# Kernel optimization log

Measured on AMD Instinct MI355X. Metric: run time of the kernel, lower is better.

## Reference

```python
import jax, jax.numpy as jnp
import numpy as np

D_MODEL = 128
NUM_HEADS = 8
LN_EPS = 1e-5


def setup_inputs() -> dict:
    key = jax.random.key(0)
    ks = jax.random.split(key, 12)
    B, T, D = 4, 2048, D_MODEL
    s = 1.0 / np.sqrt(D)
    return {
        "queries": jax.random.normal(ks[0], (B, T, D), jnp.float32),
        "keys": jax.random.normal(ks[1], (B, T, D), jnp.float32),
        "values": jax.random.normal(ks[2], (B, T, D), jnp.float32),
        "Wq": jax.random.normal(ks[3], (D, D), jnp.float32) * s,
        "bq": jnp.zeros((D,), jnp.float32),
        "Wk": jax.random.normal(ks[4], (D, D), jnp.float32) * s,
        "bk": jnp.zeros((D,), jnp.float32),
        "Wv": jax.random.normal(ks[5], (D, D), jnp.float32) * s,
        "bv": jnp.zeros((D,), jnp.float32),
        "Wo": jax.random.normal(ks[6], (D, D), jnp.float32) * s,
        "bo": jnp.zeros((D,), jnp.float32),
        "gamma": jnp.ones((D,), jnp.float32),
        "beta": jnp.zeros((D,), jnp.float32),
    }


def reference(queries, keys, values, Wq, bq, Wk, bk, Wv, bv, Wo, bo, gamma, beta):
    B, T, D = queries.shape
    H = NUM_HEADS
    dk = D // H

    def split_heads(x):  # [B,T,D] -> [B,H,T,dk]
        return x.reshape(B, -1, H, dk).transpose(0, 2, 1, 3)

    Q = split_heads(queries @ Wq + bq)
    K = split_heads(keys @ Wk + bk)
    V = split_heads(values @ Wv + bv)

    scale = 1.0 / jnp.sqrt(jnp.asarray(dk, jnp.float32))
    scores = jnp.einsum("bhqd,bhkd->bhqk", Q, K) * scale  # [B,H,T,T]
    attn = jax.nn.softmax(scores, axis=-1)
    ctx = jnp.einsum("bhqk,bhkd->bhqd", attn, V)  # [B,H,T,dk]

    out = ctx.transpose(0, 2, 1, 3).reshape(B, T, D)  # combine heads
    out = out @ Wo + bo

    x = out + queries  # residual
    mean = jnp.mean(x, axis=-1, keepdims=True)
    var = jnp.mean((x - mean) ** 2, axis=-1, keepdims=True)
    out = (x - mean) / jnp.sqrt(var + LN_EPS) * gamma + beta
    return out, attn
```

## Files before the change

### kernel.cpp

```cpp
#include <hip/hip_runtime.h>

#define B_ 4
#define T_ 2048
#define D_ 128
#define H_ 8
#define DK_ 16

typedef __attribute__((ext_vector_type(8))) short short8;
typedef __attribute__((ext_vector_type(4))) float floatx4;

__device__ __forceinline__ short f2bf(float x) {
    unsigned u = __builtin_bit_cast(unsigned, x);
    u += 0x7FFFu + ((u >> 16) & 1u);
    return (short)(u >> 16);
}

__device__ __forceinline__ unsigned cvt_pk_bf16(float lo, float hi) {
    unsigned r;
    asm("v_cvt_pk_bf16_f32 %0, %1, %2" : "=v"(r) : "v"(lo), "v"(hi));
    return r;
}

__global__ __launch_bounds__(64) void qkv_kernel(
    const float* __restrict__ q_in, const float* __restrict__ k_in,
    const float* __restrict__ v_in,
    const float* __restrict__ Wq, const float* __restrict__ bq,
    const float* __restrict__ Wk, const float* __restrict__ bk,
    const float* __restrict__ Wv, const float* __restrict__ bv,
    short* __restrict__ q_ws, short* __restrict__ k_ws, short* __restrict__ vt_ws)
{
    int mat = blockIdx.x >> 9;
    int rb  = blockIdx.x & 511;
    int row0 = rb * 16;
    int b  = row0 >> 11;
    int t0 = row0 & (T_ - 1);

    const float* X    = (mat == 0) ? q_in : (mat == 1) ? k_in : v_in;
    const float* W    = (mat == 0) ? Wq   : (mat == 1) ? Wk   : Wv;
    const float* bias = (mat == 0) ? bq   : (mat == 1) ? bk   : bv;

    __shared__ float xt[16][128];
    int tid = threadIdx.x;
    #pragma unroll
    for (int i = 0; i < 8; ++i) {
        int idx = tid + i * 64;
        int r = idx >> 5, c4 = idx & 31;
        *(float4*)&xt[r][c4 * 4] =
            *(const float4*)&X[(size_t)(row0 + r) * 128 + c4 * 4];
    }
    __syncthreads();

    int c0 = tid, c1 = tid + 64;
    float accA[16], accB[16];
    float b0 = bias[c0], b1 = bias[c1];
    #pragma unroll
    for (int r = 0; r < 16; ++r) { accA[r] = b0; accB[r] = b1; }

    for (int d4 = 0; d4 < 32; ++d4) {
        float w0[4], w1[4];
        #pragma unroll
        for (int j = 0; j < 4; ++j) {
            w0[j] = W[(d4 * 4 + j) * 128 + c0];
            w1[j] = W[(d4 * 4 + j) * 128 + c1];
        }
        #pragma unroll
        for (int r = 0; r < 16; ++r) {
            float4 xv = *(const float4*)&xt[r][d4 * 4];
            accA[r] += xv.x * w0[0] + xv.y * w0[1] + xv.z * w0[2] + xv.w * w0[3];
            accB[r] += xv.x * w1[0] + xv.y * w1[1] + xv.z * w1[2] + xv.w * w1[3];
        }
    }

    int hA = c0 >> 4, dA = c0 & 15;
    int hB = c1 >> 4, dB = c1 & 15;
    #pragma unroll
    for (int r = 0; r < 16; ++r) {
        int t = t0 + r;
        float vA = accA[r], vB = accB[r];
        if (mat == 0) { vA *= 0.25f; vB *= 0.25f; }
        if (mat == 2) {
            vt_ws[((size_t)(b * H_ + hA) * DK_ + dA) * T_ + t] = f2bf(vA);
            vt_ws[((size_t)(b * H_ + hB) * DK_ + dB) * T_ + t] = f2bf(vB);
        } else {
            short* dst = (mat == 0) ? q_ws : k_ws;
            dst[((size_t)(b * H_ + hA) * T_ + t) * DK_ + dA] = f2bf(vA);
            dst[((size_t)(b * H_ + hB) * T_ + t) * DK_ + dB] = f2bf(vB);
        }
    }
}

__global__ __launch_bounds__(512) void attn_kernel(
    const short* __restrict__ q_ws, const short* __restrict__ k_ws,
    const short* __restrict__ vt_ws,
    float* __restrict__ attn, float* __restrict__ ctx_ws)
{
    __shared__ __align__(16) short klds[T_ * DK_];
    __shared__ __align__(16) short vtlds[DK_ * (T_ + 8)];
    __shared__ __align__(16) short tblds[8 * 16 * 40];

    int tid = threadIdx.x;
    int bh = blockIdx.x >> 3;
    int qc = blockIdx.x & 7;
    int b = bh >> 3, h = bh & 7;

    const short* kbase  = k_ws  + (size_t)bh * T_ * DK_;
    const short* vtbase = vt_ws + (size_t)bh * DK_ * T_;

    #pragma unroll
    for (int i = 0; i < 8; ++i) {
        int idx = tid + i * 512;
        *(short8*)&klds[idx * 8] = *(const short8*)&kbase[idx * 8];
    }
    #pragma unroll
    for (int i = 0; i < 8; ++i) {
        int idx = tid + i * 512;
        int d = idx >> 8, off = idx & 255;
        *(short8*)&vtlds[d * (T_ + 8) + off * 8] =
            *(const short8*)&vtbase[d * T_ + off * 8];
    }
    __syncthreads();

    int wid = tid >> 6, lane = tid & 63;
    int l15 = lane & 15, quad = lane >> 4;
    int half8 = (quad & 1) * 8;
    short8 z8 = {0, 0, 0, 0, 0, 0, 0, 0};

    float* attn_bh = attn + (size_t)bh * T_ * T_;

    for (int tt = 0; tt < 2; ++tt) {
        int qrow0 = qc * 256 + tt * 128 + wid * 16;

        short8 bq = *(const short8*)
            &q_ws[((size_t)bh * T_ + qrow0 + l15) * DK_ + half8];
        if (quad >= 2) bq = z8;

        float lsum = 0.f;
        for (int tk0 = 0; tk0 < T_; tk0 += 32) {
            short8 ak0 = *(const short8*)&klds[(tk0 + l15) * DK_ + half8];
            short8 ak1 = *(const short8*)&klds[(tk0 + 16 + l15) * DK_ + half8];
            if (quad >= 2) { ak0 = z8; ak1 = z8; }
            floatx4 s0 = __builtin_amdgcn_mfma_f32_16x16x32_bf16(
                ak0, bq, (floatx4){0.f, 0.f, 0.f, 0.f}, 0, 0, 0);
            floatx4 s1 = __builtin_amdgcn_mfma_f32_16x16x32_bf16(
                ak1, bq, (floatx4){0.f, 0.f, 0.f, 0.f}, 0, 0, 0);
            #pragma unroll
            for (int r = 0; r < 4; ++r)
                lsum += __expf(s0[r]) + __expf(s1[r]);
        }
        lsum += __shfl_xor(lsum, 16);
        lsum += __shfl_xor(lsum, 32);
        float inv = 1.0f / lsum;

        short* tb = &tblds[wid * 16 * 40];
        floatx4 ctx = {0.f, 0.f, 0.f, 0.f};
        float* ap = attn_bh + (size_t)(qrow0 + l15) * T_;

        for (int tk0 = 0; tk0 < T_; tk0 += 32) {
            short8 ak0 = *(const short8*)&klds[(tk0 + l15) * DK_ + half8];
            short8 ak1 = *(const short8*)&klds[(tk0 + 16 + l15) * DK_ + half8];
            if (quad >= 2) { ak0 = z8; ak1 = z8; }
            floatx4 s0 = __builtin_amdgcn_mfma_f32_16x16x32_bf16(
                ak0, bq, (floatx4){0.f, 0.f, 0.f, 0.f}, 0, 0, 0);
            floatx4 s1 = __builtin_amdgcn_mfma_f32_16x16x32_bf16(
                ak1, bq, (floatx4){0.f, 0.f, 0.f, 0.f}, 0, 0, 0);

            float p0[4], p1[4];
            #pragma unroll
            for (int r = 0; r < 4; ++r) {
                p0[r] = __expf(s0[r]) * inv;
                p1[r] = __expf(s1[r]) * inv;
            }
            *(float4*)(ap + tk0 + quad * 4) =
                make_float4(p0[0], p0[1], p0[2], p0[3]);
            *(float4*)(ap + tk0 + 16 + quad * 4) =
                make_float4(p1[0], p1[1], p1[2], p1[3]);

            unsigned u0 = cvt_pk_bf16(p0[0], p0[1]);
            unsigned u1 = cvt_pk_bf16(p0[2], p0[3]);
            unsigned u2 = cvt_pk_bf16(p1[0], p1[1]);
            unsigned u3 = cvt_pk_bf16(p1[2], p1[3]);
            uint2 w01 = {u0, u1}, w23 = {u2, u3};
            *(uint2*)&tb[l15 * 40 + quad * 4]      = w01;
            *(uint2*)&tb[l15 * 40 + 16 + quad * 4] = w23;

            short8 pa = *(const short8*)&tb[l15 * 40 + quad * 8];
            short8 vb = *(const short8*)&vtlds[l15 * (T_ + 8) + tk0 + quad * 8];
            ctx = __builtin_amdgcn_mfma_f32_16x16x32_bf16(pa, vb, ctx, 0, 0, 0);
        }
        #pragma unroll
        for (int r = 0; r < 4; ++r)
            ctx_ws[((size_t)b * T_ + qrow0 + quad * 4 + r) * D_ + h * DK_ + l15] =
                ctx[r];
    }
}

__global__ __launch_bounds__(256) void outln_kernel(
    const float* __restrict__ ctx_ws, const float* __restrict__ Wo,
    const float* __restrict__ bo, const float* __restrict__ q_in,
    const float* __restrict__ gamma, const float* __restrict__ beta,
    float* __restrict__ out)
{
    __shared__ float xrow[4][4][128];
    int tid = threadIdx.x, wid = tid >> 6, lane = tid & 63;
    int row0 = blockIdx.x * 16 + wid * 4;

    #pragma unroll
    for (int r = 0; r < 4; ++r) {
        xrow[wid][r][lane]      = ctx_ws[(size_t)(row0 + r) * 128 + lane];
        xrow[wid][r][lane + 64] = ctx_ws[(size_t)(row0 + r) * 128 + lane + 64];
    }

    float acc0[4], acc1[4];
    float bb0 = bo[lane], bb1 = bo[lane + 64];
    #pragma unroll
    for (int r = 0; r < 4; ++r) { acc0[r] = bb0; acc1[r] = bb1; }

    for (int d4 = 0; d4 < 32; ++d4) {
        float w0[4], w1[4];
        #pragma unroll
        for (int j = 0; j < 4; ++j) {
            w0[j] = Wo[(d4 * 4 + j) * 128 + lane];
            w1[j] = Wo[(d4 * 4 + j) * 128 + lane + 64];
        }
        #pragma unroll
        for (int r = 0; r < 4; ++r) {
            float4 xv = *(const float4*)&xrow[wid][r][d4 * 4];
            acc0[r] += xv.x * w0[0] + xv.y * w0[1] + xv.z * w0[2] + xv.w * w0[3];
            acc1[r] += xv.x * w1[0] + xv.y * w1[1] + xv.z * w1[2] + xv.w * w1[3];
        }
    }

    float g0 = gamma[lane], g1 = gamma[lane + 64];
    float be0 = beta[lane], be1 = beta[lane + 64];
    #pragma unroll
    for (int r = 0; r < 4; ++r) {
        size_t row = row0 + r;
        float x0 = acc0[r] + q_in[row * 128 + lane];
        float x1 = acc1[r] + q_in[row * 128 + lane + 64];
        float s = x0 + x1, s2 = x0 * x0 + x1 * x1;
        #pragma unroll
        for (int off = 1; off < 64; off <<= 1) {
            s  += __shfl_xor(s, off);
            s2 += __shfl_xor(s2, off);
        }
        float mean = s * (1.0f / 128.0f);
        float var  = s2 * (1.0f / 128.0f) - mean * mean;
        float rstd = rsqrtf(var + 1e-5f);
        out[row * 128 + lane]      = (x0 - mean) * rstd * g0 + be0;
        out[row * 128 + lane + 64] = (x1 - mean) * rstd * g1 + be1;
    }
}

extern "C" void kernel_launch(void* const* d_in, const int* in_sizes, int n_in,
                              void* d_out, int out_size, void* d_ws, size_t ws_size,
                              hipStream_t stream)
{
    const float* queries = (const float*)d_in[0];
    const float* keys    = (const float*)d_in[1];
    const float* values  = (const float*)d_in[2];
    const float* Wq = (const float*)d_in[3];  const float* bq = (const float*)d_in[4];
    const float* Wk = (const float*)d_in[5];  const float* bk = (const float*)d_in[6];
    const float* Wv = (const float*)d_in[7];  const float* bv = (const float*)d_in[8];
    const float* Wo = (const float*)d_in[9];  const float* bo = (const float*)d_in[10];
    const float* gamma = (const float*)d_in[11];
    const float* beta  = (const float*)d_in[12];

    short* q_ws  = (short*)d_ws;
    short* k_ws  = q_ws  + (1 << 20);
    short* vt_ws = k_ws  + (1 << 20);
    float* ctx_ws = (float*)(vt_ws + (1 << 20));

    float* out  = (float*)d_out;
    float* attn = out + (size_t)B_ * T_ * D_;

    qkv_kernel<<<dim3(3 * 512), dim3(64), 0, stream>>>(
        queries, keys, values, Wq, bq, Wk, bk, Wv, bv, q_ws, k_ws, vt_ws);
    attn_kernel<<<dim3(256), dim3(512), 0, stream>>>(
        q_ws, k_ws, vt_ws, attn, ctx_ws);
    outln_kernel<<<dim3(512), dim3(256), 0, stream>>>(
        ctx_ws, Wo, bo, queries, gamma, beta, out);
}
```

Measured before the change: 623.9 us.

## Drop LDS K/V staging, double grid, swizzle blocks, use nontemporal attn stores

Removes the per-block copy of K and V^T into LDS (about 130 KB) and reads K/V straight from global memory, relying on L2/cache reuse. The grid doubles to 512 blocks with one 128-row query tile each, and launch bounds ask for 4 blocks per CU to raise occupancy. Block IDs are swizzled so neighbouring blocks spread across heads, and the large attention-matrix writes use nontemporal stores to limit cache pollution. The risk is more global/L2 traffic and load latency in the inner loops in exchange for higher occupancy.

```diff
diff --git a/kernel.cpp b/kernel.cpp
--- a/kernel.cpp
+++ b/kernel.cpp
@@ -89,36 +89,22 @@
     }
 }
 
-__global__ __launch_bounds__(512) void attn_kernel(
+__global__ __launch_bounds__(512, 4) void attn_kernel(
     const short* __restrict__ q_ws, const short* __restrict__ k_ws,
     const short* __restrict__ vt_ws,
     float* __restrict__ attn, float* __restrict__ ctx_ws)
 {
-    __shared__ __align__(16) short klds[T_ * DK_];
-    __shared__ __align__(16) short vtlds[DK_ * (T_ + 8)];
     __shared__ __align__(16) short tblds[8 * 16 * 40];
 
     int tid = threadIdx.x;
-    int bh = blockIdx.x >> 3;
-    int qc = blockIdx.x & 7;
+    int bid = blockIdx.x;
+    int wg  = ((bid & 7) << 6) | (bid >> 3);
+    int bh = wg >> 4;
+    int qc = wg & 15;
     int b = bh >> 3, h = bh & 7;
 
     const short* kbase  = k_ws  + (size_t)bh * T_ * DK_;
     const short* vtbase = vt_ws + (size_t)bh * DK_ * T_;
-
-    #pragma unroll
-    for (int i = 0; i < 8; ++i) {
-        int idx = tid + i * 512;
-        *(short8*)&klds[idx * 8] = *(const short8*)&kbase[idx * 8];
-    }
-    #pragma unroll
-    for (int i = 0; i < 8; ++i) {
-        int idx = tid + i * 512;
-        int d = idx >> 8, off = idx & 255;
-        *(short8*)&vtlds[d * (T_ + 8) + off * 8] =
-            *(const short8*)&vtbase[d * T_ + off * 8];
-    }
-    __syncthreads();
 
     int wid = tid >> 6, lane = tid & 63;
     int l15 = lane & 15, quad = lane >> 4;
@@ -126,72 +112,71 @@
     short8 z8 = {0, 0, 0, 0, 0, 0, 0, 0};
 
     float* attn_bh = attn + (size_t)bh * T_ * T_;
-
-    for (int tt = 0; tt < 2; ++tt) {
-        int qrow0 = qc * 256 + tt * 128 + wid * 16;
-
-        short8 bq = *(const short8*)
-            &q_ws[((size_t)bh * T_ + qrow0 + l15) * DK_ + half8];
-        if (quad >= 2) bq = z8;
-
-        float lsum = 0.f;
-        for (int tk0 = 0; tk0 < T_; tk0 += 32) {
-            short8 ak0 = *(const short8*)&klds[(tk0 + l15) * DK_ + half8];
-            short8 ak1 = *(const short8*)&klds[(tk0 + 16 + l15) * DK_ + half8];
-            if (quad >= 2) { ak0 = z8; ak1 = z8; }
-            floatx4 s0 = __builtin_amdgcn_mfma_f32_16x16x32_bf16(
-                ak0, bq, (floatx4){0.f, 0.f, 0.f, 0.f}, 0, 0, 0);
-            floatx4 s1 = __builtin_amdgcn_mfma_f32_16x16x32_bf16(
-                ak1, bq, (floatx4){0.f, 0.f, 0.f, 0.f}, 0, 0, 0);
-            #pragma unroll
-            for (int r = 0; r < 4; ++r)
-                lsum += __expf(s0[r]) + __expf(s1[r]);
-        }
-        lsum += __shfl_xor(lsum, 16);
-        lsum += __shfl_xor(lsum, 32);
-        float inv = 1.0f / lsum;
-
-        short* tb = &tblds[wid * 16 * 40];
-        floatx4 ctx = {0.f, 0.f, 0.f, 0.f};
-        float* ap = attn_bh + (size_t)(qrow0 + l15) * T_;
-
-        for (int tk0 = 0; tk0 < T_; tk0 += 32) {
-            short8 ak0 = *(const short8*)&klds[(tk0 + l15) * DK_ + half8];
-            short8 ak1 = *(const short8*)&klds[(tk0 + 16 + l15) * DK_ + half8];
-            if (quad >= 2) { ak0 = z8; ak1 = z8; }
-            floatx4 s0 = __builtin_amdgcn_mfma_f32_16x16x32_bf16(
-                ak0, bq, (floatx4){0.f, 0.f, 0.f, 0.f}, 0, 0, 0);
-            floatx4 s1 = __builtin_amdgcn_mfma_f32_16x16x32_bf16(
-                ak1, bq, (floatx4){0.f, 0.f, 0.f, 0.f}, 0, 0, 0);
-
-            float p0[4], p1[4];
-            #pragma unroll
-            for (int r = 0; r < 4; ++r) {
-                p0[r] = __expf(s0[r]) * inv;
-                p1[r] = __expf(s1[r]) * inv;
-            }
-            *(float4*)(ap + tk0 + quad * 4) =
-                make_float4(p0[0], p0[1], p0[2], p0[3]);
-            *(float4*)(ap + tk0 + 16 + quad * 4) =
-                make_float4(p1[0], p1[1], p1[2], p1[3]);
-
-            unsigned u0 = cvt_pk_bf16(p0[0], p0[1]);
-            unsigned u1 = cvt_pk_bf16(p0[2], p0[3]);
-            unsigned u2 = cvt_pk_bf16(p1[0], p1[1]);
-            unsigned u3 = cvt_pk_bf16(p1[2], p1[3]);
-            uint2 w01 = {u0, u1}, w23 = {u2, u3};
-            *(uint2*)&tb[l15 * 40 + quad * 4]      = w01;
-            *(uint2*)&tb[l15 * 40 + 16 + quad * 4] = w23;
-
-            short8 pa = *(const short8*)&tb[l15 * 40 + quad * 8];
-            short8 vb = *(const short8*)&vtlds[l15 * (T_ + 8) + tk0 + quad * 8];
-            ctx = __builtin_amdgcn_mfma_f32_16x16x32_bf16(pa, vb, ctx, 0, 0, 0);
-        }
+    int qrow0 = qc * 128 + wid * 16;
+
+    short8 bq = *(const short8*)
+        &q_ws[((size_t)bh * T_ + qrow0 + l15) * DK_ + half8];
+    if (quad >= 2) bq = z8;
+
+    float lsum = 0.f;
+    #pragma unroll 2
+    for (int tk0 = 0; tk0 < T_; tk0 += 32) {
+        short8 ak0 = *(const short8*)&kbase[(tk0 + l15) * DK_ + half8];
+        short8 ak1 = *(const short8*)&kbase[(tk0 + 16 + l15) * DK_ + half8];
+        if (quad >= 2) { ak0 = z8; ak1 = z8; }
+        floatx4 s0 = __builtin_amdgcn_mfma_f32_16x16x32_bf16(
+            ak0, bq, (floatx4){0.f, 0.f, 0.f, 0.f}, 0, 0, 0);
+        floatx4 s1 = __builtin_amdgcn_mfma_f32_16x16x32_bf16(
+            ak1, bq, (floatx4){0.f, 0.f, 0.f, 0.f}, 0, 0, 0);
         #pragma unroll
         for (int r = 0; r < 4; ++r)
-            ctx_ws[((size_t)b * T_ + qrow0 + quad * 4 + r) * D_ + h * DK_ + l15] =
-                ctx[r];
-    }
+            lsum += __expf(s0[r]) + __expf(s1[r]);
+    }
+    lsum += __shfl_xor(lsum, 16);
+    lsum += __shfl_xor(lsum, 32);
+    float inv = 1.0f / lsum;
+
+    short* tb = &tblds[wid * 16 * 40];
+    floatx4 ctx = {0.f, 0.f, 0.f, 0.f};
+    float* ap = attn_bh + (size_t)(qrow0 + l15) * T_;
+
+    #pragma unroll 2
+    for (int tk0 = 0; tk0 < T_; tk0 += 32) {
+        short8 ak0 = *(const short8*)&kbase[(tk0 + l15) * DK_ + half8];
+        short8 ak1 = *(const short8*)&kbase[(tk0 + 16 + l15) * DK_ + half8];
+        if (quad >= 2) { ak0 = z8; ak1 = z8; }
+        floatx4 s0 = __builtin_amdgcn_mfma_f32_16x16x32_bf16(
+            ak0, bq, (floatx4){0.f, 0.f, 0.f, 0.f}, 0, 0, 0);
+        floatx4 s1 = __builtin_amdgcn_mfma_f32_16x16x32_bf16(
+            ak1, bq, (floatx4){0.f, 0.f, 0.f, 0.f}, 0, 0, 0);
+
+        float p0[4], p1[4];
+        #pragma unroll
+        for (int r = 0; r < 4; ++r) {
+            p0[r] = __expf(s0[r]) * inv;
+            p1[r] = __expf(s1[r]) * inv;
+        }
+        floatx4 v0 = {p0[0], p0[1], p0[2], p0[3]};
+        floatx4 v1 = {p1[0], p1[1], p1[2], p1[3]};
+        __builtin_nontemporal_store(v0, (floatx4*)(ap + tk0 + quad * 4));
+        __builtin_nontemporal_store(v1, (floatx4*)(ap + tk0 + 16 + quad * 4));
+
+        unsigned u0 = cvt_pk_bf16(p0[0], p0[1]);
+        unsigned u1 = cvt_pk_bf16(p0[2], p0[3]);
+        unsigned u2 = cvt_pk_bf16(p1[0], p1[1]);
+        unsigned u3 = cvt_pk_bf16(p1[2], p1[3]);
+        uint2 w01 = {u0, u1}, w23 = {u2, u3};
+        *(uint2*)&tb[l15 * 40 + quad * 4]      = w01;
+        *(uint2*)&tb[l15 * 40 + 16 + quad * 4] = w23;
+
+        short8 pa = *(const short8*)&tb[l15 * 40 + quad * 8];
+        short8 vb = *(const short8*)&vtbase[(size_t)l15 * T_ + tk0 + quad * 8];
+        ctx = __builtin_amdgcn_mfma_f32_16x16x32_bf16(pa, vb, ctx, 0, 0, 0);
+    }
+    #pragma unroll
+    for (int r = 0; r < 4; ++r)
+        ctx_ws[((size_t)b * T_ + qrow0 + quad * 4 + r) * D_ + h * DK_ + l15] =
+            ctx[r];
 }
 
 __global__ __launch_bounds__(256) void outln_kernel(
@@ -275,7 +260,7 @@
 
     qkv_kernel<<<dim3(3 * 512), dim3(64), 0, stream>>>(
         queries, keys, values, Wq, bq, Wk, bk, Wv, bv, q_ws, k_ws, vt_ws);
-    attn_kernel<<<dim3(256), dim3(512), 0, stream>>>(
+    attn_kernel<<<dim3(512), dim3(512), 0, stream>>>(
         q_ws, k_ws, vt_ws, attn, ctx_ws);
     outln_kernel<<<dim3(512), dim3(256), 0, stream>>>(
         ctx_ws, Wo, bo, queries, gamma, beta, out);
```

After: 704.8 us. 13.0% more time.
